# Performance work log

Hardware: AMD Instinct MI355X
Metric: run time of the kernel (lower is better)

The kernel has to match this reference:

```python
import jax, jax.numpy as jnp
import numpy as np

N = 32          # objects in the (single) image
P = N * (N - 1) # relation pairs
D = 256         # self.dim
M = 14          # mask_size / pooler resolution
OC = 151        # obj classes
RC = 51         # rel classes
RED = D // 4    # attention gate reduction


def setup_inputs() -> dict:
    key = jax.random.key(0)
    ks = jax.random.split(key, 32)
    # all ordered pairs i != j
    ii, jj = np.meshgrid(np.arange(N), np.arange(N), indexing='ij')
    keep = ii != jj
    rel_pair_idxs = jnp.asarray(np.stack([ii[keep], jj[keep]], 1), jnp.int32)  # [P,2]
    # valid xyxy boxes in an 800x600 image
    x1 = jax.random.uniform(ks[0], (N,)) * 600.0
    y1 = jax.random.uniform(ks[1], (N,)) * 400.0
    w = jax.random.uniform(ks[2], (N,)) * 180.0 + 20.0
    h = jax.random.uniform(ks[3], (N,)) * 180.0 + 20.0
    bboxes = jnp.stack([x1, y1, x1 + w, y1 + h], 1).astype(jnp.float32)
    roi_features = jax.random.normal(ks[4], (N, 4096), jnp.float32)
    predict_logits = jax.random.normal(ks[5], (N, OC), jnp.float32)
    union_features = jax.random.normal(ks[6], (P, D, M, M), jnp.float32)
    s = 0.02
    p = dict(
        roi_features=roi_features, bboxes=bboxes, predict_logits=predict_logits,
        union_features=union_features, rel_pair_idxs=rel_pair_idxs,
        W_emb1=jax.random.normal(ks[7], (4096 + OC + 4, D)) * s, b_emb1=jnp.zeros((D,)),
        W_emb2=jax.random.normal(ks[8], (D, D)) * s, b_emb2=jnp.zeros((D,)),
        # stacked SE-attention gates: 0=sbj, 1=obj, 2=bg
        att_fc1_w=jax.random.normal(ks[9], (3, D, RED)) * s, att_fc1_b=jnp.zeros((3, RED)),
        att_fc2_w=jax.random.normal(ks[10], (3, RED, D)) * s, att_fc2_b=jnp.zeros((3, D)),
        W_c1=jax.random.normal(ks[11], (3 * D, D)) * s, b_c1=jnp.zeros((D,)),
        W_c2=jax.random.normal(ks[12], (D, D)) * s, b_c2=jnp.zeros((D,)),
        W_gcn=jax.random.normal(ks[13], (D, D)) * s, b_gcn=jnp.zeros((D,)),
        W_objp=jax.random.normal(ks[14], (D, OC)) * s, b_objp=jnp.zeros((OC,)),
        W_relp=jax.random.normal(ks[15], (D, RC)) * s, b_relp=jnp.zeros((RC,)),
    )
    return p


def _rect_masks(x0, y0, x1, y1):
    # mask[p, r, c] = 1 iff x0<=r<x1 and y0<=c<y1  (matches torch slice write)
    r = jnp.arange(M, dtype=jnp.float32)
    rm = (r[None, :] >= x0[:, None]) & (r[None, :] < x1[:, None])  # [P,M]
    cm = (r[None, :] >= y0[:, None]) & (r[None, :] < y1[:, None])  # [P,M]
    return (rm[:, :, None] & cm[:, None, :]).astype(jnp.float32)   # [P,M,M]


def _masking(union_features, bboxes, pairs):
    sb = bboxes[pairs[:, 0]]  # [P,4]
    ob = bboxes[pairs[:, 1]]
    ux1 = jnp.minimum(sb[:, 0], ob[:, 0])
    uy1 = jnp.minimum(sb[:, 1], ob[:, 1])
    x = jnp.stack([sb[:, 0], sb[:, 2], ob[:, 0], ob[:, 2]], 1) - ux1[:, None]
    y = jnp.stack([sb[:, 1], sb[:, 3], ob[:, 1], ob[:, 3]], 1) - uy1[:, None]
    xr = M / jnp.maximum(x[:, 1], x[:, 3])
    yr = M / jnp.maximum(y[:, 1], y[:, 3])
    xp = jnp.round(x * xr[:, None])
    yp = jnp.round(y * yr[:, None])
    sm = _rect_masks(xp[:, 0], yp[:, 0], xp[:, 1], yp[:, 1])[:, None]  # [P,1,M,M]
    om = _rect_masks(xp[:, 2], yp[:, 2], xp[:, 3], yp[:, 3])[:, None]
    bm = jnp.clip(1.0 - sm - om, 0.0, 1.0)
    return union_features * sm, union_features * om, union_features * bm


def _att_gate(x, w1, b1, w2, b2):
    # SE-style channel attention gate
    s = x.mean((2, 3))                                        # [P,D]
    g = jax.nn.sigmoid(jax.nn.relu(s @ w1 + b1) @ w2 + b2)    # [P,D]
    return x * g[:, :, None, None]


def _adjacency(pairs):
    o2o = jnp.zeros((N, N)).at[pairs[:, 0], pairs[:, 1]].set(1.0)
    ar = jnp.arange(P)
    o2r = jnp.zeros((N, P)).at[pairs[:, 0], ar].set(1.0).at[pairs[:, 1], ar].set(1.0)
    top = jnp.concatenate([o2o, o2r], 1)                     # [N, N+P]
    bot = jnp.concatenate([o2r.T, jnp.zeros((P, P))], 1)     # [P, N+P]
    adj = jnp.concatenate([top, bot], 0)
    return adj + jnp.eye(N + P)


def reference(roi_features, bboxes, predict_logits, union_features, rel_pair_idxs,
              W_emb1, b_emb1, W_emb2, b_emb2,
              att_fc1_w, att_fc1_b, att_fc2_w, att_fc2_b,
              W_c1, b_c1, W_c2, b_c2, W_gcn, b_gcn,
              W_objp, b_objp, W_relp, b_relp):
    pairs = rel_pair_idxs
    # object embedding
    obj_in = jnp.concatenate([roi_features, predict_logits, bboxes], 1)  # [N,4251]
    obj_feats = jax.nn.relu(obj_in @ W_emb1 + b_emb1) @ W_emb2 + b_emb2  # [N,D]
    # masking + attention gates + global avg pool
    sbj, obj, bg = _masking(union_features, bboxes, pairs)
    sbj = _att_gate(sbj, att_fc1_w[0], att_fc1_b[0], att_fc2_w[0], att_fc2_b[0]).mean((2, 3))
    obj = _att_gate(obj, att_fc1_w[1], att_fc1_b[1], att_fc2_w[1], att_fc2_b[1]).mean((2, 3))
    bg = _att_gate(bg, att_fc1_w[2], att_fc1_b[2], att_fc2_w[2], att_fc2_b[2]).mean((2, 3))
    # relational embedding (compose)
    rel = jnp.concatenate([sbj, obj, bg], 1)                 # [P,3D]
    rel_feats = jax.nn.relu(rel @ W_c1 + b_c1) @ W_c2 + b_c2  # [P,D]
    # GCN over object+relation graph (row-normalized adjacency, residual)
    adj = _adjacency(pairs)
    feats = jnp.concatenate([obj_feats, rel_feats], 0)        # [N+P,D]
    norm_adj = adj / adj.sum(1, keepdims=True)
    gcn_out = jax.nn.relu(norm_adj @ (feats @ W_gcn) + b_gcn) + feats
    obj_dists = gcn_out[:N] @ W_objp + b_objp                 # [N,OC]
    rel_dists = gcn_out[N:] @ W_relp + b_relp                 # [P,RC]
    return obj_dists, rel_dists
```

## Files before the change

### kernel.cpp

```cpp
#include <hip/hip_runtime.h>
#include <cstdint>
#include <cstddef>

#define NOBJ 32
#define NP   992
#define DD   256
#define SP   196
#define OC   151
#define RC   51
#define RED  64
#define KIN  4251
#define CH   128
#define KPC  34

#define OFF_PART   0u
#define OFF_OBJF   1048576u
#define OFF_SALL   1056768u
#define OFF_RELF   1818624u
#define OFF_H      2072576u
#define OFF_W2T    2334720u
#define OFF_WC1T   2400256u
#define OFF_WC2T   2596864u
#define OFF_WGT    2662400u
#define OFF_FC1WT  2727936u
#define OFF_FC2WT  2777088u
#define OFF_WOPT   2826240u
#define OFF_WRPT   2864896u

#define TR_TOT 543232

__global__ void k_pre(const float* __restrict__ uf,
                      const float* __restrict__ bbox,
                      const int* __restrict__ pairs,
                      const float* __restrict__ roi,
                      const float* __restrict__ logits,
                      const float* __restrict__ W1,
                      const float* __restrict__ W2,  const float* __restrict__ Wc1,
                      const float* __restrict__ Wc2, const float* __restrict__ Wg,
                      const float* __restrict__ f1w, const float* __restrict__ f2w,
                      const float* __restrict__ Wop, const float* __restrict__ Wrp,
                      float* __restrict__ sAll, float* __restrict__ part,
                      float* __restrict__ W2T,  float* __restrict__ Wc1T,
                      float* __restrict__ Wc2T, float* __restrict__ WgT,
                      float* __restrict__ f1wT, float* __restrict__ f2wT,
                      float* __restrict__ WopT, float* __restrict__ WrpT) {
  const int b = blockIdx.x, t = threadIdx.x;
  if (b < NP) {
    const int p = b;
    __shared__ __align__(16) float wS[SP];
    __shared__ __align__(16) float wO[SP];
    __shared__ __align__(16) float wB[SP];
    if (t < SP) {
      int si = pairs[2 * p], oi = pairs[2 * p + 1];
      float sx1 = bbox[si * 4 + 0], sy1 = bbox[si * 4 + 1];
      float sx2 = bbox[si * 4 + 2], sy2 = bbox[si * 4 + 3];
      float ox1 = bbox[oi * 4 + 0], oy1 = bbox[oi * 4 + 1];
      float ox2 = bbox[oi * 4 + 2], oy2 = bbox[oi * 4 + 3];
      float ux = fminf(sx1, ox1), uy = fminf(sy1, oy1);
      float xr = 14.f / fmaxf(sx2 - ux, ox2 - ux);
      float yr = 14.f / fmaxf(sy2 - uy, oy2 - uy);
      float xs0 = rintf((sx1 - ux) * xr), xs1 = rintf((sx2 - ux) * xr);
      float xo0 = rintf((ox1 - ux) * xr), xo1 = rintf((ox2 - ux) * xr);
      float ys0 = rintf((sy1 - uy) * yr), ys1 = rintf((sy2 - uy) * yr);
      float yo0 = rintf((oy1 - uy) * yr), yo1 = rintf((oy2 - uy) * yr);
      int a = t / 14, bb = t - a * 14;
      float fa = (float)a, fb = (float)bb;
      float sm = (fa >= xs0 && fa < xs1 && fb >= ys0 && fb < ys1) ? 1.f : 0.f;
      float om = (fa >= xo0 && fa < xo1 && fb >= yo0 && fb < yo1) ? 1.f : 0.f;
      float bm = fminf(fmaxf(1.f - sm - om, 0.f), 1.f);
      wS[t] = sm; wO[t] = om; wB[t] = bm;
    }
    __syncthreads();
    const float4* u4 = (const float4*)(uf + ((size_t)p * DD + t) * SP);
    float as0 = 0, as1 = 0, ao0 = 0, ao1 = 0, ab0 = 0, ab1 = 0;
#pragma unroll 7
    for (int j = 0; j < SP / 4; ++j) {
      float4 v  = u4[j];
      float4 ms = *(const float4*)&wS[4 * j];
      float4 mo = *(const float4*)&wO[4 * j];
      float4 mb = *(const float4*)&wB[4 * j];
      as0 += v.x * ms.x + v.y * ms.y;  as1 += v.z * ms.z + v.w * ms.w;
      ao0 += v.x * mo.x + v.y * mo.y;  ao1 += v.z * mo.z + v.w * mo.w;
      ab0 += v.x * mb.x + v.y * mb.y;  ab1 += v.z * mb.z + v.w * mb.w;
    }
    const float inv = 1.f / 196.f;
    float* o = sAll + (size_t)p * 768;
    o[t]       = (as0 + as1) * inv;
    o[256 + t] = (ao0 + ao1) * inv;
    o[512 + t] = (ab0 + ab1) * inv;
  } else if (b < NP + CH) {
    const int chunk = b - NP;
    int k0 = chunk * KPC;
    int k1 = k0 + KPC; if (k1 > KIN) k1 = KIN;
    float acc[NOBJ];
#pragma unroll
    for (int i = 0; i < NOBJ; ++i) acc[i] = 0.f;
#pragma unroll 2
    for (int k = k0; k < k1; ++k) {
      float w = W1[(size_t)k * DD + t];
      const float* xp; int stride;
      if (k < 4096)            { xp = roi    + k;               stride = 4096; }
      else if (k < 4096 + OC)  { xp = logits + (k - 4096);      stride = OC;   }
      else                     { xp = bbox   + (k - 4096 - OC); stride = 4;    }
#pragma unroll
      for (int i = 0; i < NOBJ; ++i) { acc[i] += xp[0] * w; xp += stride; }
    }
    float* pout = part + (size_t)chunk * (NOBJ * DD) + t;
#pragma unroll
    for (int i = 0; i < NOBJ; ++i) pout[i * DD] = acc[i];
  } else {
    for (int o = (b - NP - CH) * 256 + t; o < TR_TOT; o += 256 * 256) {
      float v; float* dst;
      if (o < 65536)       { int q = o;          v = W2 [(q & 255) * 256 + (q >> 8)]; dst = W2T  + q; }
      else if (o < 262144) { int q = o - 65536;  int c = q / 768, k = q - c * 768;
                             v = Wc1[k * 256 + c];                                    dst = Wc1T + q; }
      else if (o < 327680) { int q = o - 262144; v = Wc2[(q & 255) * 256 + (q >> 8)]; dst = Wc2T + q; }
      else if (o < 393216) { int q = o - 327680; v = Wg [(q & 255) * 256 + (q >> 8)]; dst = WgT  + q; }
      else if (o < 442368) { int q = o - 393216;
                             v = f1w[(q >> 14) * 16384 + (q & 255) * 64 + ((q >> 8) & 63)];
                             dst = f1wT + q; }
      else if (o < 491520) { int q = o - 442368;
                             v = f2w[(q >> 14) * 16384 + (q & 63) * 256 + ((q >> 6) & 255)];
                             dst = f2wT + q; }
      else if (o < 530176) { int q = o - 491520; v = Wop[(q & 255) * OC + (q >> 8)];  dst = WopT + q; }
      else                 { int q = o - 530176; v = Wrp[(q & 255) * RC + (q >> 8)];  dst = WrpT + q; }
      *dst = v;
    }
  }
}

__global__ void __launch_bounds__(512, 1)
k_mid2(const float* __restrict__ sAll,
       const float* __restrict__ f1wT, const float* __restrict__ f1b,
       const float* __restrict__ f2wT, const float* __restrict__ f2b,
       const float* __restrict__ Wc1T, const float* __restrict__ bc1,
       const float* __restrict__ Wc2T, const float* __restrict__ bc2,
       const float* __restrict__ WgT,
       const float* __restrict__ part, const float* __restrict__ b1,
       const float* __restrict__ W2T,  const float* __restrict__ b2,
       float* __restrict__ relf, float* __restrict__ objf,
       float* __restrict__ H) {
  const int b = blockIdx.x, t = threadIdx.x;
  const int h = t >> 8, tt = t & 255;
  __shared__ __align__(16) float sg[4][768];
  __shared__ __align__(16) float ha[4][192];
  __shared__ __align__(16) float h2[4][256];
  __shared__ __align__(16) float red[2][4][256];
  if (b < NP / 4) {
    const int p0 = b * 4;
    {
      const float4* src = (const float4*)(sAll + (size_t)p0 * 768);
      float4* dst = (float4*)&sg[0][0];
      for (int j = t; j < 768; j += 512) dst[j] = src[j];
    }
    __syncthreads();
    if (tt < 192) {
      const float4* w4 = (const float4*)(f1wT + tt * 256 + h * 128);
      const int sb = (tt >> 6) * 256 + h * 128;
      float a0 = 0, a1 = 0, a2 = 0, a3 = 0;
#pragma unroll 8
      for (int j = 0; j < 32; ++j) {
        float4 wv = w4[j];
        float4 s0 = *(const float4*)&sg[0][sb + 4 * j];
        float4 s1 = *(const float4*)&sg[1][sb + 4 * j];
        float4 s2 = *(const float4*)&sg[2][sb + 4 * j];
        float4 s3 = *(const float4*)&sg[3][sb + 4 * j];
        a0 += s0.x * wv.x + s0.y * wv.y + s0.z * wv.z + s0.w * wv.w;
        a1 += s1.x * wv.x + s1.y * wv.y + s1.z * wv.z + s1.w * wv.w;
        a2 += s2.x * wv.x + s2.y * wv.y + s2.z * wv.z + s2.w * wv.w;
        a3 += s3.x * wv.x + s3.y * wv.y + s3.z * wv.z + s3.w * wv.w;
      }
      red[h][0][tt] = a0; red[h][1][tt] = a1; red[h][2][tt] = a2; red[h][3][tt] = a3;
    }
    __syncthreads();
    if (h == 0 && tt < 192) {
      float bb = f1b[tt];
#pragma unroll
      for (int p = 0; p < 4; ++p)
        ha[p][tt] = fmaxf(red[0][p][tt] + red[1][p][tt] + bb, 0.f);
    }
    __syncthreads();
    for (int br = 0; br < 3; ++br) {
      const float4* w4 = (const float4*)(f2wT + br * 16384 + tt * 64 + h * 32);
      const int hb = br * 64 + h * 32;
      float a0 = 0, a1 = 0, a2 = 0, a3 = 0;
#pragma unroll
      for (int j = 0; j < 8; ++j) {
        float4 wv = w4[j];
        float4 v0 = *(const float4*)&ha[0][hb + 4 * j];
        float4 v1 = *(const float4*)&ha[1][hb + 4 * j];
        float4 v2 = *(const float4*)&ha[2][hb + 4 * j];
        float4 v3 = *(const float4*)&ha[3][hb + 4 * j];
        a0 += v0.x * wv.x + v0.y * wv.y + v0.z * wv.z + v0.w * wv.w;
        a1 += v1.x * wv.x + v1.y * wv.y + v1.z * wv.z + v1.w * wv.w;
        a2 += v2.x * wv.x + v2.y * wv.y + v2.z * wv.z + v2.w * wv.w;
        a3 += v3.x * wv.x + v3.y * wv.y + v3.z * wv.z + v3.w * wv.w;
      }
      red[h][0][tt] = a0; red[h][1][tt] = a1; red[h][2][tt] = a2; red[h][3][tt] = a3;
      __syncthreads();
      if (h == 0) {
        float bb = f2b[br * 256 + tt];
#pragma unroll
        for (int p = 0; p < 4; ++p) {
          float g = 1.f / (1.f + expf(-(red[0][p][tt] + red[1][p][tt] + bb)));
          sg[p][br * 256 + tt] *= g;
        }
      }
      __syncthreads();
    }
    {
      const float4* w4 = (const float4*)(Wc1T + (size_t)tt * 768 + h * 384);
      const int gb = h * 384;
      float a0 = 0, a1 = 0, a2 = 0, a3 = 0;
#pragma unroll 8
      for (int j = 0; j < 96; ++j) {
        float4 wv = w4[j];
        float4 g0 = *(const float4*)&sg[0][gb + 4 * j];
        float4 g1 = *(const float4*)&sg[1][gb + 4 * j];
        float4 g2 = *(const float4*)&sg[2][gb + 4 * j];
        float4 g3 = *(const float4*)&sg[3][gb + 4 * j];
        a0 += g0.x * wv.x + g0.y * wv.y + g0.z * wv.z + g0.w * wv.w;
        a1 += g1.x * wv.x + g1.y * wv.y + g1.z * wv.z + g1.w * wv.w;
        a2 += g2.x * wv.x + g2.y * wv.y + g2.z * wv.z + g2.w * wv.w;
        a3 += g3.x * wv.x + g3.y * wv.y + g3.z * wv.z + g3.w * wv.w;
      }
      red[h][0][tt] = a0; red[h][1][tt] = a1; red[h][2][tt] = a2; red[h][3][tt] = a3;
    }
    __syncthreads();
    if (h == 0) {
      float bb = bc1[tt];
#pragma unroll
      for (int p = 0; p < 4; ++p)
        h2[p][tt] = fmaxf(red[0][p][tt] + red[1][p][tt] + bb, 0.f);
    }
    __syncthreads();
    {
      const float4* w4 = (const float4*)(Wc2T + (size_t)tt * 256 + h * 128);
      const int hb = h * 128;
      float a0 = 0, a1 = 0, a2 = 0, a3 = 0;
#pragma unroll 8
      for (int j = 0; j < 32; ++j) {
        float4 wv = w4[j];
        float4 v0 = *(const float4*)&h2[0][hb + 4 * j];
        float4 v1 = *(const float4*)&h2[1][hb + 4 * j];
        float4 v2 = *(const float4*)&h2[2][hb + 4 * j];
        float4 v3 = *(const float4*)&h2[3][hb + 4 * j];
        a0 += v0.x * wv.x + v0.y * wv.y + v0.z * wv.z + v0.w * wv.w;
        a1 += v1.x * wv.x + v1.y * wv.y + v1.z * wv.z + v1.w * wv.w;
        a2 += v2.x * wv.x + v2.y * wv.y + v2.z * wv.z + v2.w * wv.w;
        a3 += v3.x * wv.x + v3.y * wv.y + v3.z * wv.z + v3.w * wv.w;
      }
      red[h][0][tt] = a0; red[h][1][tt] = a1; red[h][2][tt] = a2; red[h][3][tt] = a3;
    }
    __syncthreads();
    if (h == 0) {
      float bb = bc2[tt];
#pragma unroll
      for (int p = 0; p < 4; ++p) {
        float v = red[0][p][tt] + red[1][p][tt] + bb;
        relf[(size_t)(p0 + p) * DD + tt] = v;
        sg[p][tt] = v;
      }
    }
    __syncthreads();
    {
      const float4* w4 = (const float4*)(WgT + (size_t)tt * 256 + h * 128);
      const int hb = h * 128;
      float a0 = 0, a1 = 0, a2 = 0, a3 = 0;
#pragma unroll 8
      for (int j = 0; j < 32; ++j) {
        float4 wv = w4[j];
        float4 v0 = *(const float4*)&sg[0][hb + 4 * j];
        float4 v1 = *(const float4*)&sg[1][hb + 4 * j];
        float4 v2 = *(const float4*)&sg[2][hb + 4 * j];
        float4 v3 = *(const float4*)&sg[3][hb + 4 * j];
        a0 += v0.x * wv.x + v0.y * wv.y + v0.z * wv.z + v0.w * wv.w;
        a1 += v1.x * wv.x + v1.y * wv.y + v1.z * wv.z + v1.w * wv.w;
        a2 += v2.x * wv.x + v2.y * wv.y + v2.z * wv.z + v2.w * wv.w;
        a3 += v3.x * wv.x + v3.y * wv.y + v3.z * wv.z + v3.w * wv.w;
      }
      red[h][0][tt] = a0; red[h][1][tt] = a1; red[h][2][tt] = a2; red[h][3][tt] = a3;
    }
    __syncthreads();
    if (h == 0) {
#pragma unroll
      for (int p = 0; p < 4; ++p)
        H[(size_t)(NOBJ + p0 + p) * DD + tt] = red[0][p][tt] + red[1][p][tt];
    }
  } else {
    const int r = (b - NP / 4) * 2 + h;
    float s[8];
#pragma unroll
    for (int u = 0; u < 8; ++u) s[u] = 0.f;
#pragma unroll
    for (int c0 = 0; c0 < CH; c0 += 8) {
#pragma unroll
      for (int u = 0; u < 8; ++u)
        s[u] += part[(size_t)(c0 + u) * (NOBJ * DD) + r * DD + tt];
    }
    float tot = ((s[0] + s[1]) + (s[2] + s[3])) + ((s[4] + s[5]) + (s[6] + s[7]));
    h2[h][tt] = fmaxf(tot + b1[tt], 0.f);
    __syncthreads();
    {
      const float4* w4 = (const float4*)(W2T + (size_t)tt * DD);
      const float* hp = &h2[h][0];
      float a0 = 0, a1 = 0, a2 = 0, a3 = 0;
#pragma unroll 8
      for (int j = 0; j < 64; ++j) {
        float4 wv = w4[j];
        float4 hv = *(const float4*)&hp[4 * j];
        a0 += hv.x * wv.x; a1 += hv.y * wv.y; a2 += hv.z * wv.z; a3 += hv.w * wv.w;
      }
      float v = (a0 + a1) + (a2 + a3) + b2[tt];
      objf[r * DD + tt] = v;
      sg[h][tt] = v;
    }
    __syncthreads();
    {
      const float4* w4 = (const float4*)(WgT + (size_t)tt * DD);
      const float* hp = &sg[h][0];
      float a0 = 0, a1 = 0, a2 = 0, a3 = 0;
#pragma unroll 8
      for (int j = 0; j < 64; ++j) {
        float4 wv = w4[j];
        float4 hv = *(const float4*)&hp[4 * j];
        a0 += hv.x * wv.x; a1 += hv.y * wv.y; a2 += hv.z * wv.z; a3 += hv.w * wv.w;
      }
      H[(size_t)r * DD + tt] = (a0 + a1) + (a2 + a3);
    }
  }
}

__global__ void __launch_bounds__(1024, 1)
k_heads(const float* __restrict__ H, const float* __restrict__ objf,
        const float* __restrict__ relf, const int* __restrict__ pairs,
        const float* __restrict__ bg,
        const float* __restrict__ WopT, const float* __restrict__ bop,
        const float* __restrict__ WrpT, const float* __restrict__ brp,
        float* __restrict__ out) {
  const int b = blockIdx.x, t = threadIdx.x;
  const int p = t >> 8, tt = t & 255;
  if (b < NP / 4) {
    __shared__ __align__(16) float gr[4][DD];
    __shared__ float red[4][4][64];
    const int r = b * 4 + p;
    int si = pairs[2 * r], oi = pairs[2 * r + 1];
    float hsum = H[si * DD + tt] + H[oi * DD + tt] + H[(size_t)(NOBJ + r) * DD + tt];
    gr[p][tt] = fmaxf(hsum * (1.f / 3.f) + bg[tt], 0.f) + relf[(size_t)r * DD + tt];
    __syncthreads();
    const int q = tt >> 6, c = tt & 63;
    float a = 0.f;
    if (c < RC) {
      const float4* w4 = (const float4*)(WrpT + c * 256 + q * 64);
#pragma unroll
      for (int j = 0; j < 16; ++j) {
        float4 wv = w4[j];
        float4 gv = *(const float4*)&gr[p][q * 64 + 4 * j];
        a += gv.x * wv.x + gv.y * wv.y + gv.z * wv.z + gv.w * wv.w;
      }
    }
    red[p][q][c] = a;
    __syncthreads();
    if (tt < RC)
      out[NOBJ * OC + (size_t)r * RC + tt] =
          red[p][0][tt] + red[p][1][tt] + red[p][2][tt] + red[p][3][tt] + brp[tt];
  } else {
    const int i = b - NP / 4;
    const int slice = p;
    __shared__ int2 pr[NP];
    __shared__ float red2[4][DD];
    __shared__ __align__(16) float gro[DD];
    const int2* p2 = (const int2*)pairs;
    for (int r = t; r < NP; r += 1024) pr[r] = p2[r];
    __syncthreads();
    float acc = 0.f;
    if (slice == 0) {
#pragma unroll 8
      for (int j = 0; j < NOBJ; ++j) acc += H[j * DD + tt];
    }
    const int rbeg = slice * 248;
#pragma unroll 8
    for (int r = rbeg; r < rbeg + 248; ++r) {
      int2 q = pr[r];
      float v = H[(size_t)(NOBJ + r) * DD + tt];
      if (q.x == i || q.y == i) acc += v;
    }
    red2[slice][tt] = acc;
    __syncthreads();
    if (t < DD) {
      float pre = (red2[0][t] + red2[1][t] + red2[2][t] + red2[3][t]) * (1.f / 94.f);
      gro[t] = fmaxf(pre + bg[t], 0.f) + objf[i * DD + t];
    }
    __syncthreads();
    float hsum = 0.f;
    if (tt < OC) {
      const float4* w4 = (const float4*)(WopT + tt * 256 + slice * 64);
#pragma unroll
      for (int j = 0; j < 16; ++j) {
        float4 wv = w4[j];
        float4 gv = *(const float4*)&gro[slice * 64 + 4 * j];
        hsum += gv.x * wv.x + gv.y * wv.y + gv.z * wv.z + gv.w * wv.w;
      }
    }
    red2[slice][tt] = hsum;
    __syncthreads();
    if (t < OC)
      out[i * OC + t] = red2[0][t] + red2[1][t] + red2[2][t] + red2[3][t] + bop[t];
  }
}

extern "C" void kernel_launch(void* const* d_in, const int* in_sizes, int n_in,
                              void* d_out, int out_size, void* d_ws, size_t ws_size,
                              hipStream_t stream) {
  const float* roi   = (const float*)d_in[0];
  const float* bbox  = (const float*)d_in[1];
  const float* logit = (const float*)d_in[2];
  const float* uf    = (const float*)d_in[3];
  const int*   pairs = (const int*)d_in[4];
  const float* W1    = (const float*)d_in[5];
  const float* b1    = (const float*)d_in[6];
  const float* W2    = (const float*)d_in[7];
  const float* b2    = (const float*)d_in[8];
  const float* fc1w  = (const float*)d_in[9];
  const float* fc1b  = (const float*)d_in[10];
  const float* fc2w  = (const float*)d_in[11];
  const float* fc2b  = (const float*)d_in[12];
  const float* Wc1   = (const float*)d_in[13];
  const float* bc1   = (const float*)d_in[14];
  const float* Wc2   = (const float*)d_in[15];
  const float* bc2   = (const float*)d_in[16];
  const float* Wg    = (const float*)d_in[17];
  const float* bg    = (const float*)d_in[18];
  const float* Wop   = (const float*)d_in[19];
  const float* bop   = (const float*)d_in[20];
  const float* Wrp   = (const float*)d_in[21];
  const float* brp   = (const float*)d_in[22];

  float* ws    = (float*)d_ws;
  float* part  = ws + OFF_PART;
  float* objf  = ws + OFF_OBJF;
  float* sAll  = ws + OFF_SALL;
  float* relf  = ws + OFF_RELF;
  float* Hbuf  = ws + OFF_H;
  float* W2T   = ws + OFF_W2T;
  float* Wc1T  = ws + OFF_WC1T;
  float* Wc2T  = ws + OFF_WC2T;
  float* WgT   = ws + OFF_WGT;
  float* f1wT  = ws + OFF_FC1WT;
  float* f2wT  = ws + OFF_FC2WT;
  float* WopT  = ws + OFF_WOPT;
  float* WrpT  = ws + OFF_WRPT;
  float* out   = (float*)d_out;

  k_pre<<<NP + CH + 256, 256, 0, stream>>>(uf, bbox, pairs, roi, logit, W1,
                                           W2, Wc1, Wc2, Wg, fc1w, fc2w, Wop, Wrp,
                                           sAll, part, W2T, Wc1T, Wc2T, WgT,
                                           f1wT, f2wT, WopT, WrpT);
  k_mid2<<<NP / 4 + 16, 512, 0, stream>>>(sAll, f1wT, fc1b, f2wT, fc2b,
                                          Wc1T, bc1, Wc2T, bc2, WgT,
                                          part, b1, W2T, b2, relf, objf, Hbuf);
  k_heads<<<NP / 4 + NOBJ, 1024, 0, stream>>>(Hbuf, objf, relf, pairs, bg,
                                              WopT, bop, WrpT, brp, out);
}
```

Before: 525.9 us.

## Stage union-feature channels through LDS with coalesced loads in masked pooling

The masked-pooling blocks previously had each thread stream its own 196-float channel row, so neighbouring lanes read addresses far apart. The new code copies 64-channel tiles into shared memory with contiguous float4 loads, then has four threads per channel reduce 52-element slices and combine the partial sums through a small shared buffer. This targets the uncoalesced global reads on the dominant 200MB input. In exchange it uses about 52KB of LDS per block, which lowers occupancy, adds several barriers per tile, and the staging loop does not overlap loads with compute.

```diff
diff --git a/kernel.cpp b/kernel.cpp
--- a/kernel.cpp
+++ b/kernel.cpp
@@ -47,9 +47,11 @@
   const int b = blockIdx.x, t = threadIdx.x;
   if (b < NP) {
     const int p = b;
-    __shared__ __align__(16) float wS[SP];
-    __shared__ __align__(16) float wO[SP];
-    __shared__ __align__(16) float wB[SP];
+    __shared__ __align__(16) float tile[64 * SP + 64];
+    __shared__ __align__(16) float wS[256];
+    __shared__ __align__(16) float wO[256];
+    __shared__ __align__(16) float wB[256];
+    __shared__ float pacc[3][4][64];
     if (t < SP) {
       int si = pairs[2 * p], oi = pairs[2 * p + 1];
       float sx1 = bbox[si * 4 + 0], sy1 = bbox[si * 4 + 1];
@@ -69,25 +71,43 @@
       float om = (fa >= xo0 && fa < xo1 && fb >= yo0 && fb < yo1) ? 1.f : 0.f;
       float bm = fminf(fmaxf(1.f - sm - om, 0.f), 1.f);
       wS[t] = sm; wO[t] = om; wB[t] = bm;
-    }
-    __syncthreads();
-    const float4* u4 = (const float4*)(uf + ((size_t)p * DD + t) * SP);
-    float as0 = 0, as1 = 0, ao0 = 0, ao1 = 0, ab0 = 0, ab1 = 0;
-#pragma unroll 7
-    for (int j = 0; j < SP / 4; ++j) {
-      float4 v  = u4[j];
-      float4 ms = *(const float4*)&wS[4 * j];
-      float4 mo = *(const float4*)&wO[4 * j];
-      float4 mb = *(const float4*)&wB[4 * j];
-      as0 += v.x * ms.x + v.y * ms.y;  as1 += v.z * ms.z + v.w * ms.w;
-      ao0 += v.x * mo.x + v.y * mo.y;  ao1 += v.z * mo.z + v.w * mo.w;
-      ab0 += v.x * mb.x + v.y * mb.y;  ab1 += v.z * mb.z + v.w * mb.w;
-    }
+    } else {
+      wS[t] = 0.f; wO[t] = 0.f; wB[t] = 0.f;
+    }
+    if (t < 64) tile[64 * SP + t] = 0.f;
+    __syncthreads();
+    const int c = t >> 2, q = t & 3;
+    const float* row = tile + c * SP + q * 52;
+    const float* mS = wS + q * 52;
+    const float* mO = wO + q * 52;
+    const float* mB = wB + q * 52;
     const float inv = 1.f / 196.f;
-    float* o = sAll + (size_t)p * 768;
-    o[t]       = (as0 + as1) * inv;
-    o[256 + t] = (ao0 + ao1) * inv;
-    o[512 + t] = (ab0 + ab1) * inv;
+#pragma unroll 1
+    for (int ti = 0; ti < 4; ++ti) {
+      const float4* src4 = (const float4*)(uf + (size_t)p * (DD * SP) + ti * (64 * SP));
+      float4* dst4 = (float4*)tile;
+      for (int f = t; f < 64 * SP / 4; f += 256) dst4[f] = src4[f];
+      __syncthreads();
+      float a0 = 0.f, a1 = 0.f, a2 = 0.f;
+#pragma unroll
+      for (int g = 0; g < 13; ++g) {
+        float4 v  = *(const float4*)&row[4 * g];
+        float4 ms = *(const float4*)&mS[4 * g];
+        float4 mo = *(const float4*)&mO[4 * g];
+        float4 mb = *(const float4*)&mB[4 * g];
+        a0 += v.x * ms.x + v.y * ms.y + v.z * ms.z + v.w * ms.w;
+        a1 += v.x * mo.x + v.y * mo.y + v.z * mo.z + v.w * mo.w;
+        a2 += v.x * mb.x + v.y * mb.y + v.z * mb.z + v.w * mb.w;
+      }
+      pacc[0][q][c] = a0; pacc[1][q][c] = a1; pacc[2][q][c] = a2;
+      __syncthreads();
+      if (t < 192) {
+        int m = t >> 6, c2 = t & 63;
+        float s = pacc[m][0][c2] + pacc[m][1][c2] + pacc[m][2][c2] + pacc[m][3][c2];
+        sAll[(size_t)p * 768 + m * 256 + ti * 64 + c2] = s * inv;
+      }
+      __syncthreads();
+    }
   } else if (b < NP + CH) {
     const int chunk = b - NP;
     int k0 = chunk * KPC;
```

New measurement: 521.3 us. About the same (-0.9%).
